# Kernel tuning notes

Measured on AMD Instinct MI355X. Metric: run time of the kernel, lower is better.

## Reference

```python
import jax, jax.numpy as jnp
import numpy as np

H = 2048   # hidden_size
V = 50257  # output_size (vocab)


def setup_inputs() -> dict:
    key = jax.random.key(0)
    ks = jax.random.split(key, 8)
    s = 1.0 / np.sqrt(H)
    return {
        "word":   jax.random.normal(ks[0], (H,), dtype=jnp.float32),
        "hidden": jax.random.normal(ks[1], (1, 1, H), dtype=jnp.float32),
        "w_ih":   jax.random.uniform(ks[2], (3 * H, H), jnp.float32, -s, s),
        "w_hh":   jax.random.uniform(ks[3], (3 * H, H), jnp.float32, -s, s),
        "b_ih":   jax.random.uniform(ks[4], (3 * H,), jnp.float32, -s, s),
        "b_hh":   jax.random.uniform(ks[5], (3 * H,), jnp.float32, -s, s),
        "lin_w":  jax.random.uniform(ks[6], (V, H), jnp.float32, -s, s),
        "lin_b":  jax.random.uniform(ks[7], (V,), jnp.float32, -s, s),
    }


def reference(word, hidden, w_ih, w_hh, b_ih, b_hh, lin_w, lin_b):
    h0 = hidden.reshape(-1)                      # (H,)
    gi = w_ih @ word + b_ih                      # (3H,) input gates
    gh = w_hh @ h0 + b_hh                        # (3H,) hidden gates
    i_r, i_z, i_n = gi[:H], gi[H:2 * H], gi[2 * H:]
    h_r, h_z, h_n = gh[:H], gh[H:2 * H], gh[2 * H:]
    r = jax.nn.sigmoid(i_r + h_r)
    z = jax.nn.sigmoid(i_z + h_z)
    n = jnp.tanh(i_n + r * h_n)
    h_new = ((1.0 - z) * n + z * h0).reshape(1, 1, H)
    # NOTE: original computes probs from the OLD hidden, not h_new
    logits = hidden @ lin_w.T + lin_b            # (1,1,V)
    probs = jax.nn.softmax(logits, axis=-1)
    return (probs, h_new)
```

## Files before the change

### kernel.cpp

```cpp
#include <hip/hip_runtime.h>
#include <hip/hip_bf16.h>
#include <math.h>

#define H 2048
#define V 50257
#define G3H (3 * H)

__global__ __launch_bounds__(256) void gru_matvec_kernel(
    const float* __restrict__ word, const float* __restrict__ h0,
    const float* __restrict__ w_ih, const float* __restrict__ w_hh,
    const float* __restrict__ b_ih, const float* __restrict__ b_hh,
    float* __restrict__ gi, float* __restrict__ gh) {
    const int wid_in_blk = threadIdx.x >> 6;
    const int lane = threadIdx.x & 63;
    const int row = blockIdx.x * 4 + wid_in_blk;
    if (row >= G3H) return;

    const float4* wi = reinterpret_cast<const float4*>(w_ih + (size_t)row * H);
    const float4* wh = reinterpret_cast<const float4*>(w_hh + (size_t)row * H);
    const float4* x4 = reinterpret_cast<const float4*>(word);
    const float4* h4 = reinterpret_cast<const float4*>(h0);

    float acc_i = 0.f, acc_h = 0.f;
    #pragma unroll
    for (int k = lane; k < H / 4; k += 64) {
        float4 a = wi[k];
        float4 x = x4[k];
        acc_i += a.x * x.x + a.y * x.y + a.z * x.z + a.w * x.w;
        float4 b = wh[k];
        float4 h = h4[k];
        acc_h += b.x * h.x + b.y * h.y + b.z * h.z + b.w * h.w;
    }
    #pragma unroll
    for (int off = 32; off > 0; off >>= 1) {
        acc_i += __shfl_down(acc_i, off, 64);
        acc_h += __shfl_down(acc_h, off, 64);
    }
    if (lane == 0) {
        gi[row] = acc_i + b_ih[row];
        gh[row] = acc_h + b_hh[row];
    }
}

__global__ __launch_bounds__(256) void gru_gate_kernel(
    const float* __restrict__ gi, const float* __restrict__ gh,
    const float* __restrict__ h0, float* __restrict__ out_hnew) {
    int j = blockIdx.x * blockDim.x + threadIdx.x;
    if (j >= H) return;
    float r = 1.f / (1.f + expf(-(gi[j] + gh[j])));
    float z = 1.f / (1.f + expf(-(gi[H + j] + gh[H + j])));
    float n = tanhf(gi[2 * H + j] + r * gh[2 * H + j]);
    out_hnew[j] = (1.f - z) * n + z * h0[j];
}

__global__ __launch_bounds__(256) void logits_kernel(
    const float* __restrict__ lin_w, const float* __restrict__ lin_b,
    const float* __restrict__ h0, float* __restrict__ logits) {
    const int wid_in_blk = threadIdx.x >> 6;
    const int lane = threadIdx.x & 63;
    const int row = blockIdx.x * 4 + wid_in_blk;
    if (row >= V) return;

    const float4* w4 = reinterpret_cast<const float4*>(lin_w + (size_t)row * H);
    const float4* h4 = reinterpret_cast<const float4*>(h0);

    float acc = 0.f;
    #pragma unroll
    for (int k = lane; k < H / 4; k += 64) {
        float4 a = w4[k];
        float4 h = h4[k];
        acc += a.x * h.x + a.y * h.y + a.z * h.z + a.w * h.w;
    }
    #pragma unroll
    for (int off = 32; off > 0; off >>= 1) acc += __shfl_down(acc, off, 64);
    if (lane == 0) logits[row] = acc + lin_b[row];
}

__global__ __launch_bounds__(1024) void softmax_reduce_kernel(
    const float* __restrict__ logits, float* __restrict__ scalars) {
    __shared__ float red_m[16];
    __shared__ float red_s[16];
    const int tid = threadIdx.x;
    const int lane = tid & 63;
    const int wid = tid >> 6;
    const int nthreads = 1024;

    float m = -INFINITY;
    for (int v = tid; v < V; v += nthreads) m = fmaxf(m, logits[v]);
    #pragma unroll
    for (int off = 32; off > 0; off >>= 1) m = fmaxf(m, __shfl_down(m, off, 64));
    if (lane == 0) red_m[wid] = m;
    __syncthreads();
    if (wid == 0) {
        float mm = (lane < 16) ? red_m[lane] : -INFINITY;
        #pragma unroll
        for (int off = 32; off > 0; off >>= 1) mm = fmaxf(mm, __shfl_down(mm, off, 64));
        if (lane == 0) red_m[0] = mm;
    }
    __syncthreads();
    const float gmax = red_m[0];

    float s = 0.f;
    for (int v = tid; v < V; v += nthreads) s += expf(logits[v] - gmax);
    #pragma unroll
    for (int off = 32; off > 0; off >>= 1) s += __shfl_down(s, off, 64);
    if (lane == 0) red_s[wid] = s;
    __syncthreads();
    if (wid == 0) {
        float ss = (lane < 16) ? red_s[lane] : 0.f;
        #pragma unroll
        for (int off = 32; off > 0; off >>= 1) ss += __shfl_down(ss, off, 64);
        if (lane == 0) {
            scalars[0] = gmax;
            scalars[1] = 1.f / ss;
        }
    }
}

__global__ __launch_bounds__(256) void probs_kernel(
    const float* __restrict__ logits, const float* __restrict__ scalars,
    float* __restrict__ out_probs) {
    int v = blockIdx.x * blockDim.x + threadIdx.x;
    if (v >= V) return;
    out_probs[v] = expf(logits[v] - scalars[0]) * scalars[1];
}

extern "C" void kernel_launch(void* const* d_in, const int* in_sizes, int n_in,
                              void* d_out, int out_size, void* d_ws, size_t ws_size,
                              hipStream_t stream) {
    const float* word = (const float*)d_in[0];
    const float* hidden = (const float*)d_in[1];
    const float* w_ih = (const float*)d_in[2];
    const float* w_hh = (const float*)d_in[3];
    const float* b_ih = (const float*)d_in[4];
    const float* b_hh = (const float*)d_in[5];
    const float* lin_w = (const float*)d_in[6];
    const float* lin_b = (const float*)d_in[7];

    float* out = (float*)d_out;
    float* ws = (float*)d_ws;
    float* gi = ws;
    float* gh = ws + G3H;
    float* logits = ws + 2 * G3H;
    float* scalars = ws + 2 * G3H + V + 15;

    gru_matvec_kernel<<<G3H / 4, 256, 0, stream>>>(word, hidden, w_ih, w_hh,
                                                   b_ih, b_hh, gi, gh);
    logits_kernel<<<(V + 3) / 4, 256, 0, stream>>>(lin_w, lin_b, hidden, logits);
    gru_gate_kernel<<<(H + 255) / 256, 256, 0, stream>>>(gi, gh, hidden, out + V);
    softmax_reduce_kernel<<<1, 1024, 0, stream>>>(logits, scalars);
    probs_kernel<<<(V + 255) / 256, 256, 0, stream>>>(logits, scalars, out);
}
```

Measured before the change: 109.9 us.

## Fuse GRU gates into matvec, multi-row logits, and parallel two-pass softmax

Merges the GRU matvec and gate kernels into one kernel in which six waves compute the ih and hh dot products for four hidden units and one thread per unit applies the gates, which removes the gi/gh round trip and one launch. The logits and GRU matvecs now make each wave handle four rows, loading each input-vector chunk once for all four and reading the weights with nontemporal loads. The single-block softmax reduction becomes a 128-block partial max/sum, and the probs kernel merges those partials with an online-softmax combine in every block. This takes the serial one-block reduction off the critical path, at the cost of every probs block redoing the small combine.

```diff
diff --git a/kernel.cpp b/kernel.cpp
--- a/kernel.cpp
+++ b/kernel.cpp
@@ -4,125 +4,176 @@
 
 #define H 2048
 #define V 50257
-#define G3H (3 * H)
-
-__global__ __launch_bounds__(256) void gru_matvec_kernel(
+#define KV4 (H / 4)
+#define NBSM 128
+
+typedef float f4 __attribute__((ext_vector_type(4)));
+
+__device__ __forceinline__ f4 ntload(const f4* p) {
+    return __builtin_nontemporal_load(p);
+}
+
+__device__ __forceinline__ float wave_reduce_sum(float x) {
+    #pragma unroll
+    for (int off = 32; off; off >>= 1) x += __shfl_down(x, off, 64);
+    return x;
+}
+
+__device__ __forceinline__ float wave_allreduce_max(float x) {
+    #pragma unroll
+    for (int off = 32; off; off >>= 1) x = fmaxf(x, __shfl_xor(x, off, 64));
+    return x;
+}
+
+__global__ __launch_bounds__(384) void gru_fused_kernel(
     const float* __restrict__ word, const float* __restrict__ h0,
     const float* __restrict__ w_ih, const float* __restrict__ w_hh,
     const float* __restrict__ b_ih, const float* __restrict__ b_hh,
-    float* __restrict__ gi, float* __restrict__ gh) {
-    const int wid_in_blk = threadIdx.x >> 6;
+    float* __restrict__ out_hnew) {
+    __shared__ float red[6][4];
     const int lane = threadIdx.x & 63;
-    const int row = blockIdx.x * 4 + wid_in_blk;
-    if (row >= G3H) return;
-
-    const float4* wi = reinterpret_cast<const float4*>(w_ih + (size_t)row * H);
-    const float4* wh = reinterpret_cast<const float4*>(w_hh + (size_t)row * H);
-    const float4* x4 = reinterpret_cast<const float4*>(word);
-    const float4* h4 = reinterpret_cast<const float4*>(h0);
-
-    float acc_i = 0.f, acc_h = 0.f;
-    #pragma unroll
-    for (int k = lane; k < H / 4; k += 64) {
-        float4 a = wi[k];
-        float4 x = x4[k];
-        acc_i += a.x * x.x + a.y * x.y + a.z * x.z + a.w * x.w;
-        float4 b = wh[k];
-        float4 h = h4[k];
-        acc_h += b.x * h.x + b.y * h.y + b.z * h.z + b.w * h.w;
-    }
-    #pragma unroll
-    for (int off = 32; off > 0; off >>= 1) {
-        acc_i += __shfl_down(acc_i, off, 64);
-        acc_h += __shfl_down(acc_h, off, 64);
-    }
+    const int w = threadIdx.x >> 6;
+    const int j0 = blockIdx.x * 4;
+    const int gate = (w < 3) ? w : (w - 3);
+    const float* W = (w < 3) ? w_ih : w_hh;
+    const f4* vec = reinterpret_cast<const f4*>((w < 3) ? word : h0);
+
+    const size_t rb = (size_t)(gate * H + j0) * H;
+    const f4* r0 = reinterpret_cast<const f4*>(W + rb);
+    const f4* r1 = reinterpret_cast<const f4*>(W + rb + H);
+    const f4* r2 = reinterpret_cast<const f4*>(W + rb + 2 * H);
+    const f4* r3 = reinterpret_cast<const f4*>(W + rb + 3 * H);
+
+    float a0 = 0.f, a1 = 0.f, a2 = 0.f, a3 = 0.f;
+    #pragma unroll 4
+    for (int k = lane; k < KV4; k += 64) {
+        f4 x = vec[k];
+        f4 p0 = ntload(&r0[k]);
+        a0 += p0.x * x.x + p0.y * x.y + p0.z * x.z + p0.w * x.w;
+        f4 p1 = ntload(&r1[k]);
+        a1 += p1.x * x.x + p1.y * x.y + p1.z * x.z + p1.w * x.w;
+        f4 p2 = ntload(&r2[k]);
+        a2 += p2.x * x.x + p2.y * x.y + p2.z * x.z + p2.w * x.w;
+        f4 p3 = ntload(&r3[k]);
+        a3 += p3.x * x.x + p3.y * x.y + p3.z * x.z + p3.w * x.w;
+    }
+    a0 = wave_reduce_sum(a0);
+    a1 = wave_reduce_sum(a1);
+    a2 = wave_reduce_sum(a2);
+    a3 = wave_reduce_sum(a3);
     if (lane == 0) {
-        gi[row] = acc_i + b_ih[row];
-        gh[row] = acc_h + b_hh[row];
-    }
-}
-
-__global__ __launch_bounds__(256) void gru_gate_kernel(
-    const float* __restrict__ gi, const float* __restrict__ gh,
-    const float* __restrict__ h0, float* __restrict__ out_hnew) {
-    int j = blockIdx.x * blockDim.x + threadIdx.x;
-    if (j >= H) return;
-    float r = 1.f / (1.f + expf(-(gi[j] + gh[j])));
-    float z = 1.f / (1.f + expf(-(gi[H + j] + gh[H + j])));
-    float n = tanhf(gi[2 * H + j] + r * gh[2 * H + j]);
-    out_hnew[j] = (1.f - z) * n + z * h0[j];
+        red[w][0] = a0; red[w][1] = a1; red[w][2] = a2; red[w][3] = a3;
+    }
+    __syncthreads();
+    if (threadIdx.x < 4) {
+        const int jj = threadIdx.x;
+        const int j = j0 + jj;
+        float ir = red[0][jj] + b_ih[j];
+        float iz = red[1][jj] + b_ih[H + j];
+        float in_ = red[2][jj] + b_ih[2 * H + j];
+        float hr = red[3][jj] + b_hh[j];
+        float hz = red[4][jj] + b_hh[H + j];
+        float hn = red[5][jj] + b_hh[2 * H + j];
+        float r = 1.f / (1.f + expf(-(ir + hr)));
+        float z = 1.f / (1.f + expf(-(iz + hz)));
+        float n = tanhf(in_ + r * hn);
+        out_hnew[j] = (1.f - z) * n + z * h0[j];
+    }
 }
 
 __global__ __launch_bounds__(256) void logits_kernel(
     const float* __restrict__ lin_w, const float* __restrict__ lin_b,
     const float* __restrict__ h0, float* __restrict__ logits) {
-    const int wid_in_blk = threadIdx.x >> 6;
     const int lane = threadIdx.x & 63;
-    const int row = blockIdx.x * 4 + wid_in_blk;
-    if (row >= V) return;
-
-    const float4* w4 = reinterpret_cast<const float4*>(lin_w + (size_t)row * H);
-    const float4* h4 = reinterpret_cast<const float4*>(h0);
-
-    float acc = 0.f;
-    #pragma unroll
-    for (int k = lane; k < H / 4; k += 64) {
-        float4 a = w4[k];
-        float4 h = h4[k];
-        acc += a.x * h.x + a.y * h.y + a.z * h.z + a.w * h.w;
-    }
-    #pragma unroll
-    for (int off = 32; off > 0; off >>= 1) acc += __shfl_down(acc, off, 64);
-    if (lane == 0) logits[row] = acc + lin_b[row];
-}
-
-__global__ __launch_bounds__(1024) void softmax_reduce_kernel(
-    const float* __restrict__ logits, float* __restrict__ scalars) {
-    __shared__ float red_m[16];
-    __shared__ float red_s[16];
+    const int wid = threadIdx.x >> 6;
+    const int row0 = (blockIdx.x * 4 + wid) * 4;
+    const int q0 = min(row0 + 0, V - 1);
+    const int q1 = min(row0 + 1, V - 1);
+    const int q2 = min(row0 + 2, V - 1);
+    const int q3 = min(row0 + 3, V - 1);
+    const f4* w0 = reinterpret_cast<const f4*>(lin_w + (size_t)q0 * H);
+    const f4* w1 = reinterpret_cast<const f4*>(lin_w + (size_t)q1 * H);
+    const f4* w2 = reinterpret_cast<const f4*>(lin_w + (size_t)q2 * H);
+    const f4* w3 = reinterpret_cast<const f4*>(lin_w + (size_t)q3 * H);
+    const f4* h4 = reinterpret_cast<const f4*>(h0);
+
+    float a0 = 0.f, a1 = 0.f, a2 = 0.f, a3 = 0.f;
+    #pragma unroll 4
+    for (int k = lane; k < KV4; k += 64) {
+        f4 h = h4[k];
+        f4 p0 = ntload(&w0[k]);
+        a0 += p0.x * h.x + p0.y * h.y + p0.z * h.z + p0.w * h.w;
+        f4 p1 = ntload(&w1[k]);
+        a1 += p1.x * h.x + p1.y * h.y + p1.z * h.z + p1.w * h.w;
+        f4 p2 = ntload(&w2[k]);
+        a2 += p2.x * h.x + p2.y * h.y + p2.z * h.z + p2.w * h.w;
+        f4 p3 = ntload(&w3[k]);
+        a3 += p3.x * h.x + p3.y * h.y + p3.z * h.z + p3.w * h.w;
+    }
+    a0 = wave_reduce_sum(a0);
+    a1 = wave_reduce_sum(a1);
+    a2 = wave_reduce_sum(a2);
+    a3 = wave_reduce_sum(a3);
+    if (lane == 0) {
+        if (row0 + 0 < V) logits[row0 + 0] = a0 + lin_b[row0 + 0];
+        if (row0 + 1 < V) logits[row0 + 1] = a1 + lin_b[row0 + 1];
+        if (row0 + 2 < V) logits[row0 + 2] = a2 + lin_b[row0 + 2];
+        if (row0 + 3 < V) logits[row0 + 3] = a3 + lin_b[row0 + 3];
+    }
+}
+
+__global__ __launch_bounds__(256) void softmax_partial_kernel(
+    const float* __restrict__ logits, float* __restrict__ pm,
+    float* __restrict__ ps) {
+    __shared__ float rm[4], rs[4];
     const int tid = threadIdx.x;
     const int lane = tid & 63;
     const int wid = tid >> 6;
-    const int nthreads = 1024;
+    const int chunk = (V + NBSM - 1) / NBSM;
+    const int start = blockIdx.x * chunk;
+    const int end = min(V, start + chunk);
 
     float m = -INFINITY;
-    for (int v = tid; v < V; v += nthreads) m = fmaxf(m, logits[v]);
-    #pragma unroll
-    for (int off = 32; off > 0; off >>= 1) m = fmaxf(m, __shfl_down(m, off, 64));
-    if (lane == 0) red_m[wid] = m;
-    __syncthreads();
-    if (wid == 0) {
-        float mm = (lane < 16) ? red_m[lane] : -INFINITY;
+    for (int v = start + tid; v < end; v += 256) m = fmaxf(m, logits[v]);
+    m = wave_allreduce_max(m);
+    if (lane == 0) rm[wid] = m;
+    __syncthreads();
+    m = fmaxf(fmaxf(rm[0], rm[1]), fmaxf(rm[2], rm[3]));
+
+    float s = 0.f;
+    for (int v = start + tid; v < end; v += 256) s += expf(logits[v] - m);
+    s = wave_reduce_sum(s);
+    if (lane == 0) rs[wid] = s;
+    __syncthreads();
+    if (tid == 0) {
+        pm[blockIdx.x] = m;
+        ps[blockIdx.x] = rs[0] + rs[1] + rs[2] + rs[3];
+    }
+}
+
+__global__ __launch_bounds__(256) void probs_kernel(
+    const float* __restrict__ logits, const float* __restrict__ pm,
+    const float* __restrict__ ps, float* __restrict__ out_probs) {
+    __shared__ float sM, sInvS;
+    if (threadIdx.x < 64) {
+        const int lane = threadIdx.x;
+        float m0 = pm[lane], s0 = ps[lane];
+        float m1 = pm[lane + 64], s1 = ps[lane + 64];
+        float M = fmaxf(m0, m1);
+        float S = s0 * expf(m0 - M) + s1 * expf(m1 - M);
         #pragma unroll
-        for (int off = 32; off > 0; off >>= 1) mm = fmaxf(mm, __shfl_down(mm, off, 64));
-        if (lane == 0) red_m[0] = mm;
-    }
-    __syncthreads();
-    const float gmax = red_m[0];
-
-    float s = 0.f;
-    for (int v = tid; v < V; v += nthreads) s += expf(logits[v] - gmax);
-    #pragma unroll
-    for (int off = 32; off > 0; off >>= 1) s += __shfl_down(s, off, 64);
-    if (lane == 0) red_s[wid] = s;
-    __syncthreads();
-    if (wid == 0) {
-        float ss = (lane < 16) ? red_s[lane] : 0.f;
-        #pragma unroll
-        for (int off = 32; off > 0; off >>= 1) ss += __shfl_down(ss, off, 64);
-        if (lane == 0) {
-            scalars[0] = gmax;
-            scalars[1] = 1.f / ss;
+        for (int off = 32; off; off >>= 1) {
+            float Mo = __shfl_xor(M, off, 64);
+            float So = __shfl_xor(S, off, 64);
+            float Mn = fmaxf(M, Mo);
+            S = S * expf(M - Mn) + So * expf(Mo - Mn);
+            M = Mn;
         }
-    }
-}
-
-__global__ __launch_bounds__(256) void probs_kernel(
-    const float* __restrict__ logits, const float* __restrict__ scalars,
-    float* __restrict__ out_probs) {
-    int v = blockIdx.x * blockDim.x + threadIdx.x;
-    if (v >= V) return;
-    out_probs[v] = expf(logits[v] - scalars[0]) * scalars[1];
+        if (lane == 0) { sM = M; sInvS = 1.f / S; }
+    }
+    __syncthreads();
+    const int v = blockIdx.x * 256 + threadIdx.x;
+    if (v < V) out_probs[v] = expf(logits[v] - sM) * sInvS;
 }
 
 extern "C" void kernel_launch(void* const* d_in, const int* in_sizes, int n_in,
@@ -139,15 +190,13 @@
 
     float* out = (float*)d_out;
     float* ws = (float*)d_ws;
-    float* gi = ws;
-    float* gh = ws + G3H;
-    float* logits = ws + 2 * G3H;
-    float* scalars = ws + 2 * G3H + V + 15;
-
-    gru_matvec_kernel<<<G3H / 4, 256, 0, stream>>>(word, hidden, w_ih, w_hh,
-                                                   b_ih, b_hh, gi, gh);
-    logits_kernel<<<(V + 3) / 4, 256, 0, stream>>>(lin_w, lin_b, hidden, logits);
-    gru_gate_kernel<<<(H + 255) / 256, 256, 0, stream>>>(gi, gh, hidden, out + V);
-    softmax_reduce_kernel<<<1, 1024, 0, stream>>>(logits, scalars);
-    probs_kernel<<<(V + 255) / 256, 256, 0, stream>>>(logits, scalars, out);
-}
+    float* logits = ws;
+    float* pm = ws + V + 64;
+    float* ps = pm + NBSM;
+
+    logits_kernel<<<(V + 15) / 16, 256, 0, stream>>>(lin_w, lin_b, hidden, logits);
+    gru_fused_kernel<<<H / 4, 384, 0, stream>>>(word, hidden, w_ih, w_hh,
+                                                b_ih, b_hh, out + V);
+    softmax_partial_kernel<<<NBSM, 256, 0, stream>>>(logits, pm, ps);
+    probs_kernel<<<(V + 255) / 256, 256, 0, stream>>>(logits, pm, ps, out);
+}
```

Measured after the change: 103.9 us. 5.4% less time.
